# Performance work log

Hardware: AMD Instinct MI355X
Metric: run time of the kernel (lower is better)

The kernel has to match this reference:

```python
import jax, jax.numpy as jnp
import numpy as np

D_MODEL = 1024
N_HEADS = 16
D_K = D_MODEL // N_HEADS
B, S = 2, 2048


def setup_inputs() -> dict:
    key = jax.random.key(0)
    ks = jax.random.split(key, 5)
    x = jax.random.normal(ks[0], (B, S, D_MODEL), dtype=jnp.float32)
    # causal 0/1 mask, broadcastable over batch and heads
    mask = jnp.tril(jnp.ones((S, S), dtype=jnp.int32))[None, None, :, :]
    scale = 1.0 / np.sqrt(D_MODEL)
    w_qkv_w = jax.random.normal(ks[1], (3 * D_MODEL, D_MODEL), dtype=jnp.float32) * scale
    w_qkv_b = jnp.zeros((3 * D_MODEL,), dtype=jnp.float32)
    w_o_w = jax.random.normal(ks[2], (D_MODEL, D_MODEL), dtype=jnp.float32) * scale
    w_o_b = jnp.zeros((D_MODEL,), dtype=jnp.float32)
    return {"x": x, "mask": mask, "w_qkv_w": w_qkv_w, "w_qkv_b": w_qkv_b,
            "w_o_w": w_o_w, "w_o_b": w_o_b}


def reference(x, mask, w_qkv_w, w_qkv_b, w_o_w, w_o_b):
    b, s, d = x.shape
    qkv = x @ w_qkv_w.T + w_qkv_b                       # [b, s, 3d]
    q, k, v = jnp.split(qkv, 3, axis=-1)
    # [b, h, s, dk]
    q = q.reshape(b, s, N_HEADS, D_K).transpose(0, 2, 1, 3)
    k = k.reshape(b, s, N_HEADS, D_K).transpose(0, 2, 1, 3)
    v = v.reshape(b, s, N_HEADS, D_K).transpose(0, 2, 1, 3)
    scores = jnp.einsum('bhqd,bhkd->bhqk', q, k) / jnp.sqrt(jnp.float32(D_K))
    scores = jnp.where(mask == 0, jnp.float32(-1e9), scores)
    attn = jax.nn.softmax(scores, axis=-1)
    out = jnp.einsum('bhqk,bhkd->bhqd', attn, v)        # [b, h, s, dk]
    out = out.transpose(0, 2, 1, 3).reshape(b, s, d)
    return out @ w_o_w.T + w_o_b
```

## Files before the change

### kernel.cpp

```cpp
#include <hip/hip_runtime.h>
#include <cstdint>
#include <cstddef>


typedef __attribute__((ext_vector_type(8))) short bf16x8;
typedef __attribute__((ext_vector_type(4))) float f32x4;
typedef __attribute__((ext_vector_type(4))) unsigned int u32x4;
typedef __attribute__((ext_vector_type(4))) unsigned short u16x4;
typedef __attribute__((ext_vector_type(8))) unsigned short u16x8;

__device__ __forceinline__ unsigned short f2b(float f) {
  unsigned int u = __float_as_uint(f);
  u = u + 0x7FFFu + ((u >> 16) & 1u);
  return (unsigned short)(u >> 16);
}
__device__ __forceinline__ unsigned short f2b_trunc(float f) {
  return (unsigned short)(__float_as_uint(f) >> 16);
}

__device__ __forceinline__ void gl_lds16(const unsigned short* g, unsigned short* s) {
  __builtin_amdgcn_global_load_lds((const __attribute__((address_space(1))) void*)g,
                                   (__attribute__((address_space(3))) void*)s, 16, 0, 0);
}

__global__ __launch_bounds__(256) void cvt_all(const float* __restrict__ x,
                                               const float* __restrict__ wq,
                                               const float* __restrict__ wo,
                                               unsigned short* __restrict__ xb,
                                               unsigned short* __restrict__ wqb,
                                               unsigned short* __restrict__ wob) {
  const int bid = blockIdx.x;
  const float* in;
  unsigned short* out;
  int base;
  if (bid < 4096)      { in = x;  out = xb;  base = bid; }
  else if (bid < 7168) { in = wq; out = wqb; base = bid - 4096; }
  else                 { in = wo; out = wob; base = bid - 7168; }
  const int idx = (base * 256 + threadIdx.x) * 4;
  f32x4 v = *(const f32x4*)(in + idx);
  u16x4 r;
  r[0] = f2b(v[0]); r[1] = f2b(v[1]); r[2] = f2b(v[2]); r[3] = f2b(v[3]);
  *(u16x4*)(out + idx) = r;
}

__global__ __launch_bounds__(256) void gemm_bt(const unsigned short* __restrict__ A,
                                               const unsigned short* __restrict__ W,
                                               const float* __restrict__ bias,
                                               unsigned short* __restrict__ Cb,
                                               int M, int N, int K, int qcols) {
  __shared__ unsigned short As[128 * 32];
  __shared__ unsigned short Bs[128 * 32];
  const int tid  = threadIdx.x;
  const int lane = tid & 63;
  const int w    = tid >> 6;
  const int wy   = w >> 1, wx = w & 1;
  const int l15  = lane & 15, quad = lane >> 4;
  const int m0 = blockIdx.y * 128, n0 = blockIdx.x * 128;

  const int c0 = tid, c1 = tid + 256;
  const unsigned short* gA0 = A + (size_t)(m0 + (c0 >> 2)) * K + (c0 & 3) * 8;
  const unsigned short* gA1 = A + (size_t)(m0 + (c1 >> 2)) * K + (c1 & 3) * 8;
  const unsigned short* gB0 = W + (size_t)(n0 + (c0 >> 2)) * K + (c0 & 3) * 8;
  const unsigned short* gB1 = W + (size_t)(n0 + (c1 >> 2)) * K + (c1 & 3) * 8;
  unsigned short* sA0 = &As[c0 * 8];
  unsigned short* sA1 = &As[c1 * 8];
  unsigned short* sB0 = &Bs[c0 * 8];
  unsigned short* sB1 = &Bs[c1 * 8];

  f32x4 acc[4][4];
#pragma unroll
  for (int i = 0; i < 4; ++i)
#pragma unroll
    for (int j = 0; j < 4; ++j) acc[i][j] = (f32x4){0.f, 0.f, 0.f, 0.f};

  for (int kt = 0; kt < K; kt += 32) {
    gl_lds16(gA0 + kt, sA0);
    gl_lds16(gA1 + kt, sA1);
    gl_lds16(gB0 + kt, sB0);
    gl_lds16(gB1 + kt, sB1);
    __syncthreads();
    bf16x8 af[4], bfr[4];
#pragma unroll
    for (int i = 0; i < 4; ++i)
      af[i] = *(const bf16x8*)&As[(wy * 64 + i * 16 + l15) * 32 + quad * 8];
#pragma unroll
    for (int j = 0; j < 4; ++j)
      bfr[j] = *(const bf16x8*)&Bs[(wx * 64 + j * 16 + l15) * 32 + quad * 8];
#pragma unroll
    for (int i = 0; i < 4; ++i)
#pragma unroll
      for (int j = 0; j < 4; ++j)
        acc[i][j] = __builtin_amdgcn_mfma_f32_16x16x32_bf16(af[i], bfr[j], acc[i][j], 0, 0, 0);
    __syncthreads();
  }

#pragma unroll
  for (int i = 0; i < 4; ++i) {
    const int row = m0 + wy * 64 + i * 16 + quad * 4;
#pragma unroll
    for (int j = 0; j < 4; ++j) {
      const int col = n0 + wx * 64 + j * 16 + l15;
      const float bv = bias[col];
      const float sc = (col < qcols) ? 0.125f : 1.0f;
#pragma unroll
      for (int r = 0; r < 4; ++r)
        Cb[(size_t)(row + r) * N + col] = f2b((acc[i][j][r] + bv) * sc);
    }
  }
}

__global__ __launch_bounds__(256) void gemm_bt64(const unsigned short* __restrict__ A,
                                                 const unsigned short* __restrict__ W,
                                                 const float* __restrict__ bias,
                                                 float* __restrict__ Cf,
                                                 int M, int N, int K) {
  __shared__ unsigned short As[64 * 32];
  __shared__ unsigned short Bs[128 * 32];
  const int tid  = threadIdx.x;
  const int lane = tid & 63;
  const int w    = tid >> 6;
  const int wy   = w >> 1, wx = w & 1;
  const int l15  = lane & 15, quad = lane >> 4;
  const int m0 = blockIdx.y * 64, n0 = blockIdx.x * 128;

  const int c0 = tid, c1 = tid + 256;
  const unsigned short* gA0 = A + (size_t)(m0 + (c0 >> 2)) * K + (c0 & 3) * 8;
  const unsigned short* gB0 = W + (size_t)(n0 + (c0 >> 2)) * K + (c0 & 3) * 8;
  const unsigned short* gB1 = W + (size_t)(n0 + (c1 >> 2)) * K + (c1 & 3) * 8;
  unsigned short* sA0 = &As[c0 * 8];
  unsigned short* sB0 = &Bs[c0 * 8];
  unsigned short* sB1 = &Bs[c1 * 8];

  f32x4 acc[2][4];
#pragma unroll
  for (int i = 0; i < 2; ++i)
#pragma unroll
    for (int j = 0; j < 4; ++j) acc[i][j] = (f32x4){0.f, 0.f, 0.f, 0.f};

  for (int kt = 0; kt < K; kt += 32) {
    gl_lds16(gA0 + kt, sA0);
    gl_lds16(gB0 + kt, sB0);
    gl_lds16(gB1 + kt, sB1);
    __syncthreads();
    bf16x8 af[2], bfr[4];
#pragma unroll
    for (int i = 0; i < 2; ++i)
      af[i] = *(const bf16x8*)&As[(wy * 32 + i * 16 + l15) * 32 + quad * 8];
#pragma unroll
    for (int j = 0; j < 4; ++j)
      bfr[j] = *(const bf16x8*)&Bs[(wx * 64 + j * 16 + l15) * 32 + quad * 8];
#pragma unroll
    for (int i = 0; i < 2; ++i)
#pragma unroll
      for (int j = 0; j < 4; ++j)
        acc[i][j] = __builtin_amdgcn_mfma_f32_16x16x32_bf16(af[i], bfr[j], acc[i][j], 0, 0, 0);
    __syncthreads();
  }

#pragma unroll
  for (int i = 0; i < 2; ++i) {
    const int row = m0 + wy * 32 + i * 16 + quad * 4;
#pragma unroll
    for (int j = 0; j < 4; ++j) {
      const int col = n0 + wx * 64 + j * 16 + l15;
      const float bv = bias[col];
#pragma unroll
      for (int r = 0; r < 4; ++r)
        Cf[(size_t)(row + r) * N + col] = acc[i][j][r] + bv;
    }
  }
}

__global__ __launch_bounds__(256) void transpose_v(const unsigned short* __restrict__ qkv,
                                                   unsigned short* __restrict__ vt) {
  __shared__ unsigned short tile[64][72];
  const int tid = threadIdx.x;
  const int bh = blockIdx.y, b = bh >> 4, h = bh & 15;
  const int s0 = blockIdx.x * 64;
  const int i = tid >> 2;
  const int j = (tid & 3) * 16;
  const unsigned short* g = qkv + (size_t)(b * 2048 + s0 + i) * 3072 + 2048 + h * 64 + j;
  *(u32x4*)&tile[i][j]     = *(const u32x4*)g;
  *(u32x4*)&tile[i][j + 8] = *(const u32x4*)(g + 8);
  __syncthreads();
  const int d  = tid >> 2;
  const int sj = (tid & 3) * 16;
  u16x8 o0, o1;
#pragma unroll
  for (int k = 0; k < 8; ++k) { o0[k] = tile[sj + k][d]; o1[k] = tile[sj + 8 + k][d]; }
  unsigned short* gout = vt + (size_t)(bh * 64 + d) * 2048 + s0 + sj;
  *(u16x8*)gout       = o0;
  *(u16x8*)(gout + 8) = o1;
}

__global__ __launch_bounds__(256) void attn_fwd(const unsigned short* __restrict__ qkv,
                                                const unsigned short* __restrict__ vt,
                                                unsigned short* __restrict__ o) {
  __shared__ unsigned short Ks[2][64 * 72];
  __shared__ unsigned short Vs[2][64 * 72];
  __shared__ unsigned short pbuf[4][16 * 72];
  const int tid  = threadIdx.x;
  const int lane = tid & 63;
  const int w    = tid >> 6;
  const int l15  = lane & 15, quad = lane >> 4;
  const int bh = blockIdx.x, b = bh >> 4, h = bh & 15;
  const int qtile = 31 - (int)blockIdx.y;
  const int q0 = qtile * 64 + w * 16;
  const int T = qtile + 1;

  const int srow = tid >> 2;
  const int scol = (tid & 3) * 16;
  const unsigned short* gK = qkv + (size_t)(b * 2048 + srow) * 3072 + 1024 + h * 64 + scol;
  const unsigned short* gV = vt + (size_t)(bh * 64 + srow) * 2048 + scol;

  const unsigned short* qbase = qkv + (size_t)(b * 2048 + q0 + l15) * 3072 + h * 64;
  const bf16x8 aq0 = *(const bf16x8*)(qbase + quad * 8);
  const bf16x8 aq1 = *(const bf16x8*)(qbase + 32 + quad * 8);

  bf16x8 vones;
#pragma unroll
  for (int k = 0; k < 8; ++k) vones[k] = (short)0x3F80;

  f32x4 acc[4];
#pragma unroll
  for (int j = 0; j < 4; ++j) acc[j] = (f32x4){0.f, 0.f, 0.f, 0.f};
  f32x4 accL = (f32x4){0.f, 0.f, 0.f, 0.f};

  unsigned short* P = pbuf[w];

  {
    u32x4 k0 = *(const u32x4*)gK, k1 = *(const u32x4*)(gK + 8);
    u32x4 v0 = *(const u32x4*)gV, v1 = *(const u32x4*)(gV + 8);
    unsigned short* sK = &Ks[0][srow * 72 + scol];
    unsigned short* sV = &Vs[0][srow * 72 + scol];
    *(u32x4*)sK = k0; *(u32x4*)(sK + 8) = k1;
    *(u32x4*)sV = v0; *(u32x4*)(sV + 8) = v1;
  }

  for (int t = 0; t < T; ++t) {
    __syncthreads();
    const int cur = t & 1;
    const unsigned short* Kc = Ks[cur];
    const unsigned short* Vc = Vs[cur];
    u32x4 nk0, nk1, nv0, nv1;
    const bool more = (t + 1 < T);
    if (more) {
      const size_t ko = (size_t)(t + 1) * 64 * 3072;
      const int vo = (t + 1) * 64;
      nk0 = *(const u32x4*)(gK + ko); nk1 = *(const u32x4*)(gK + ko + 8);
      nv0 = *(const u32x4*)(gV + vo); nv1 = *(const u32x4*)(gV + vo + 8);
    }
    const int kv0 = t * 64;
    f32x4 s[4];
#pragma unroll
    for (int n = 0; n < 4; ++n) {
      const bf16x8 bk0 = *(const bf16x8*)&Kc[(n * 16 + l15) * 72 + quad * 8];
      const bf16x8 bk1 = *(const bf16x8*)&Kc[(n * 16 + l15) * 72 + 32 + quad * 8];
      f32x4 z = (f32x4){0.f, 0.f, 0.f, 0.f};
      z = __builtin_amdgcn_mfma_f32_16x16x32_bf16(aq0, bk0, z, 0, 0, 0);
      z = __builtin_amdgcn_mfma_f32_16x16x32_bf16(aq1, bk1, z, 0, 0, 0);
      s[n] = z;
    }
    if (kv0 + 63 > q0) {
#pragma unroll
      for (int n = 0; n < 4; ++n)
#pragma unroll
        for (int r = 0; r < 4; ++r)
          if (kv0 + n * 16 + l15 > q0 + quad * 4 + r) s[n][r] = -1e30f;
    }
#pragma unroll
    for (int n = 0; n < 4; ++n)
#pragma unroll
      for (int r = 0; r < 4; ++r) s[n][r] = __expf(s[n][r]);
#pragma unroll
    for (int n = 0; n < 4; ++n)
#pragma unroll
      for (int r = 0; r < 4; ++r)
        P[(quad * 4 + r) * 72 + n * 16 + l15] = f2b_trunc(s[n][r]);
    const bf16x8 ap0 = *(const bf16x8*)&P[l15 * 72 + quad * 8];
    const bf16x8 ap1 = *(const bf16x8*)&P[l15 * 72 + 32 + quad * 8];
#pragma unroll
    for (int j = 0; j < 4; ++j) {
      const bf16x8 bv0 = *(const bf16x8*)&Vc[(j * 16 + l15) * 72 + quad * 8];
      const bf16x8 bv1 = *(const bf16x8*)&Vc[(j * 16 + l15) * 72 + 32 + quad * 8];
      acc[j] = __builtin_amdgcn_mfma_f32_16x16x32_bf16(ap0, bv0, acc[j], 0, 0, 0);
      acc[j] = __builtin_amdgcn_mfma_f32_16x16x32_bf16(ap1, bv1, acc[j], 0, 0, 0);
    }
    accL = __builtin_amdgcn_mfma_f32_16x16x32_bf16(ap0, vones, accL, 0, 0, 0);
    accL = __builtin_amdgcn_mfma_f32_16x16x32_bf16(ap1, vones, accL, 0, 0, 0);
    if (more) {
      unsigned short* sK = &Ks[cur ^ 1][srow * 72 + scol];
      unsigned short* sV = &Vs[cur ^ 1][srow * 72 + scol];
      *(u32x4*)sK = nk0; *(u32x4*)(sK + 8) = nk1;
      *(u32x4*)sV = nv0; *(u32x4*)(sV + 8) = nv1;
    }
  }
#pragma unroll
  for (int j = 0; j < 4; ++j)
#pragma unroll
    for (int r = 0; r < 4; ++r) {
      const float v = acc[j][r] / accL[r];
      o[(size_t)(b * 2048 + q0 + quad * 4 + r) * 1024 + h * 64 + j * 16 + l15] = f2b(v);
    }
}

extern "C" void kernel_launch(void* const* d_in, const int* in_sizes, int n_in,
                              void* d_out, int out_size, void* d_ws, size_t ws_size,
                              hipStream_t stream) {
  const float* x       = (const float*)d_in[0];
  const float* w_qkv_w = (const float*)d_in[2];
  const float* w_qkv_b = (const float*)d_in[3];
  const float* w_o_w   = (const float*)d_in[4];
  const float* w_o_b   = (const float*)d_in[5];
  float* out = (float*)d_out;

  unsigned short* ws    = (unsigned short*)d_ws;
  unsigned short* xb    = ws;
  unsigned short* wqb   = xb   + (size_t)4096 * 1024;
  unsigned short* wob   = wqb  + (size_t)3072 * 1024;
  unsigned short* qkvb  = wob  + (size_t)1024 * 1024;
  unsigned short* vtb   = qkvb + (size_t)4096 * 3072;
  unsigned short* attnb = vtb  + (size_t)2048 * 2048;

  cvt_all<<<8192, 256, 0, stream>>>(x, w_qkv_w, w_o_w, xb, wqb, wob);
  gemm_bt<<<dim3(24, 32), 256, 0, stream>>>(xb, wqb, w_qkv_b, qkvb, 4096, 3072, 1024, 1024);
  transpose_v<<<dim3(32, 32), 256, 0, stream>>>(qkvb, vtb);
  attn_fwd<<<dim3(32, 32), 256, 0, stream>>>(qkvb, vtb, attnb);
  gemm_bt64<<<dim3(8, 64), 256, 0, stream>>>(attnb, wob, w_o_b, out, 4096, 1024, 1024);
}
```

Before: 214.7 us.

## Double GEMM K-tile to 64 with XOR-swizzled LDS layout

Both projection GEMM kernels now stage a 64-wide K slice per iteration instead of 32, which halves the number of barrier pairs and loop iterations. The LDS tiles are stored with an XOR swizzle of the 16-byte chunk index by row, applied on the global source side, so the fragment reads avoid bank conflicts. In exchange the kernels use twice the shared memory per block, which may reduce occupancy, and each thread issues more loads per iteration.

```diff
diff --git a/kernel.cpp b/kernel.cpp
--- a/kernel.cpp
+++ b/kernel.cpp
@@ -48,24 +48,30 @@
                                                const float* __restrict__ bias,
                                                unsigned short* __restrict__ Cb,
                                                int M, int N, int K, int qcols) {
-  __shared__ unsigned short As[128 * 32];
-  __shared__ unsigned short Bs[128 * 32];
+  __shared__ unsigned short As[128 * 64];
+  __shared__ unsigned short Bs[128 * 64];
   const int tid  = threadIdx.x;
   const int lane = tid & 63;
   const int w    = tid >> 6;
   const int wy   = w >> 1, wx = w & 1;
   const int l15  = lane & 15, quad = lane >> 4;
+  const int xr   = l15 & 7;
   const int m0 = blockIdx.y * 128, n0 = blockIdx.x * 128;
 
-  const int c0 = tid, c1 = tid + 256;
-  const unsigned short* gA0 = A + (size_t)(m0 + (c0 >> 2)) * K + (c0 & 3) * 8;
-  const unsigned short* gA1 = A + (size_t)(m0 + (c1 >> 2)) * K + (c1 & 3) * 8;
-  const unsigned short* gB0 = W + (size_t)(n0 + (c0 >> 2)) * K + (c0 & 3) * 8;
-  const unsigned short* gB1 = W + (size_t)(n0 + (c1 >> 2)) * K + (c1 & 3) * 8;
-  unsigned short* sA0 = &As[c0 * 8];
-  unsigned short* sA1 = &As[c1 * 8];
-  unsigned short* sB0 = &Bs[c0 * 8];
-  unsigned short* sB1 = &Bs[c1 * 8];
+  const unsigned short* gA[4];
+  const unsigned short* gB[4];
+  unsigned short* sA[4];
+  unsigned short* sB[4];
+#pragma unroll
+  for (int p = 0; p < 4; ++p) {
+    const int c = tid + p * 256;
+    const int r = c >> 3;
+    const int srcc = (c & 7) ^ (r & 7);
+    gA[p] = A + (size_t)(m0 + r) * K + srcc * 8;
+    gB[p] = W + (size_t)(n0 + r) * K + srcc * 8;
+    sA[p] = &As[c * 8];
+    sB[p] = &Bs[c * 8];
+  }
 
   f32x4 acc[4][4];
 #pragma unroll
@@ -73,24 +79,28 @@
 #pragma unroll
     for (int j = 0; j < 4; ++j) acc[i][j] = (f32x4){0.f, 0.f, 0.f, 0.f};
 
-  for (int kt = 0; kt < K; kt += 32) {
-    gl_lds16(gA0 + kt, sA0);
-    gl_lds16(gA1 + kt, sA1);
-    gl_lds16(gB0 + kt, sB0);
-    gl_lds16(gB1 + kt, sB1);
-    __syncthreads();
-    bf16x8 af[4], bfr[4];
-#pragma unroll
-    for (int i = 0; i < 4; ++i)
-      af[i] = *(const bf16x8*)&As[(wy * 64 + i * 16 + l15) * 32 + quad * 8];
-#pragma unroll
-    for (int j = 0; j < 4; ++j)
-      bfr[j] = *(const bf16x8*)&Bs[(wx * 64 + j * 16 + l15) * 32 + quad * 8];
-#pragma unroll
-    for (int i = 0; i < 4; ++i)
+  for (int kt = 0; kt < K; kt += 64) {
+#pragma unroll
+    for (int p = 0; p < 4; ++p) {
+      gl_lds16(gA[p] + kt, sA[p]);
+      gl_lds16(gB[p] + kt, sB[p]);
+    }
+    __syncthreads();
+#pragma unroll
+    for (int kc = 0; kc < 2; ++kc) {
+      bf16x8 af[4], bfr[4];
+#pragma unroll
+      for (int i = 0; i < 4; ++i)
+        af[i] = *(const bf16x8*)&As[(wy * 64 + i * 16 + l15) * 64 + ((kc * 4 + quad) ^ xr) * 8];
 #pragma unroll
       for (int j = 0; j < 4; ++j)
-        acc[i][j] = __builtin_amdgcn_mfma_f32_16x16x32_bf16(af[i], bfr[j], acc[i][j], 0, 0, 0);
+        bfr[j] = *(const bf16x8*)&Bs[(wx * 64 + j * 16 + l15) * 64 + ((kc * 4 + quad) ^ xr) * 8];
+#pragma unroll
+      for (int i = 0; i < 4; ++i)
+#pragma unroll
+        for (int j = 0; j < 4; ++j)
+          acc[i][j] = __builtin_amdgcn_mfma_f32_16x16x32_bf16(af[i], bfr[j], acc[i][j], 0, 0, 0);
+    }
     __syncthreads();
   }
 
@@ -114,22 +124,36 @@
                                                  const float* __restrict__ bias,
                                                  float* __restrict__ Cf,
                                                  int M, int N, int K) {
-  __shared__ unsigned short As[64 * 32];
-  __shared__ unsigned short Bs[128 * 32];
+  __shared__ unsigned short As[64 * 64];
+  __shared__ unsigned short Bs[128 * 64];
   const int tid  = threadIdx.x;
   const int lane = tid & 63;
   const int w    = tid >> 6;
   const int wy   = w >> 1, wx = w & 1;
   const int l15  = lane & 15, quad = lane >> 4;
+  const int xr   = l15 & 7;
   const int m0 = blockIdx.y * 64, n0 = blockIdx.x * 128;
 
-  const int c0 = tid, c1 = tid + 256;
-  const unsigned short* gA0 = A + (size_t)(m0 + (c0 >> 2)) * K + (c0 & 3) * 8;
-  const unsigned short* gB0 = W + (size_t)(n0 + (c0 >> 2)) * K + (c0 & 3) * 8;
-  const unsigned short* gB1 = W + (size_t)(n0 + (c1 >> 2)) * K + (c1 & 3) * 8;
-  unsigned short* sA0 = &As[c0 * 8];
-  unsigned short* sB0 = &Bs[c0 * 8];
-  unsigned short* sB1 = &Bs[c1 * 8];
+  const unsigned short* gA[2];
+  const unsigned short* gB[4];
+  unsigned short* sA[2];
+  unsigned short* sB[4];
+#pragma unroll
+  for (int p = 0; p < 2; ++p) {
+    const int c = tid + p * 256;
+    const int r = c >> 3;
+    const int srcc = (c & 7) ^ (r & 7);
+    gA[p] = A + (size_t)(m0 + r) * K + srcc * 8;
+    sA[p] = &As[c * 8];
+  }
+#pragma unroll
+  for (int p = 0; p < 4; ++p) {
+    const int c = tid + p * 256;
+    const int r = c >> 3;
+    const int srcc = (c & 7) ^ (r & 7);
+    gB[p] = W + (size_t)(n0 + r) * K + srcc * 8;
+    sB[p] = &Bs[c * 8];
+  }
 
   f32x4 acc[2][4];
 #pragma unroll
@@ -137,23 +161,27 @@
 #pragma unroll
     for (int j = 0; j < 4; ++j) acc[i][j] = (f32x4){0.f, 0.f, 0.f, 0.f};
 
-  for (int kt = 0; kt < K; kt += 32) {
-    gl_lds16(gA0 + kt, sA0);
-    gl_lds16(gB0 + kt, sB0);
-    gl_lds16(gB1 + kt, sB1);
-    __syncthreads();
-    bf16x8 af[2], bfr[4];
-#pragma unroll
-    for (int i = 0; i < 2; ++i)
-      af[i] = *(const bf16x8*)&As[(wy * 32 + i * 16 + l15) * 32 + quad * 8];
-#pragma unroll
-    for (int j = 0; j < 4; ++j)
-      bfr[j] = *(const bf16x8*)&Bs[(wx * 64 + j * 16 + l15) * 32 + quad * 8];
-#pragma unroll
-    for (int i = 0; i < 2; ++i)
+  for (int kt = 0; kt < K; kt += 64) {
+#pragma unroll
+    for (int p = 0; p < 2; ++p) gl_lds16(gA[p] + kt, sA[p]);
+#pragma unroll
+    for (int p = 0; p < 4; ++p) gl_lds16(gB[p] + kt, sB[p]);
+    __syncthreads();
+#pragma unroll
+    for (int kc = 0; kc < 2; ++kc) {
+      bf16x8 af[2], bfr[4];
+#pragma unroll
+      for (int i = 0; i < 2; ++i)
+        af[i] = *(const bf16x8*)&As[(wy * 32 + i * 16 + l15) * 64 + ((kc * 4 + quad) ^ xr) * 8];
 #pragma unroll
       for (int j = 0; j < 4; ++j)
-        acc[i][j] = __builtin_amdgcn_mfma_f32_16x16x32_bf16(af[i], bfr[j], acc[i][j], 0, 0, 0);
+        bfr[j] = *(const bf16x8*)&Bs[(wx * 64 + j * 16 + l15) * 64 + ((kc * 4 + quad) ^ xr) * 8];
+#pragma unroll
+      for (int i = 0; i < 2; ++i)
+#pragma unroll
+        for (int j = 0; j < 4; ++j)
+          acc[i][j] = __builtin_amdgcn_mfma_f32_16x16x32_bf16(af[i], bfr[j], acc[i][j], 0, 0, 0);
+    }
     __syncthreads();
   }
 
```

Result: faster. 198.9 us (-7.4%).
